# Kernel tuning notes

Measured on AMD Instinct MI355X. Metric: run time of the kernel, lower is better.

The kernel has to match this reference:

```python
import jax, jax.numpy as jnp
import numpy as np

N, B, C, H = 2048, 2, 1024, 16
HD = C // H


def setup_inputs() -> dict:
    key = jax.random.key(0)
    ks = jax.random.split(key, 11)
    s = 0.02
    return {
        "query": jax.random.normal(ks[0], (N, B, C), jnp.float32),
        "key": jax.random.normal(ks[1], (N, B, C), jnp.float32),
        "value": jax.random.normal(ks[2], (B, N, C), jnp.float32),
        "num_heads": H,
        "Wq": jax.random.normal(ks[3], (C, C), jnp.float32) * s,
        "bq": jnp.zeros((C,), jnp.float32),
        "Wk": jax.random.normal(ks[4], (C, HD), jnp.float32) * s,
        "bk": jnp.zeros((HD,), jnp.float32),
        "Wv": jax.random.normal(ks[5], (C, HD), jnp.float32) * s,
        "bv": jnp.zeros((HD,), jnp.float32),
        "Wp": jax.random.normal(ks[6], (C, C), jnp.float32) * s,
        "bp": jnp.zeros((C,), jnp.float32),
    }


def reference(query, key, value, num_heads, Wq, bq, Wk, bk, Wv, bv, Wp, bp):
    # query/key arrive seq-first (N,B,C); permute to batch-first as in torch code
    k_in = jnp.transpose(key, (1, 0, 2))    # (B, Nk, C)
    q_in = jnp.transpose(query, (1, 0, 2))  # (B, Nq, C)
    Bsz, Nq, Cd = q_in.shape
    hd = Cd // num_heads
    scale = hd ** -0.5

    # shared single K/V head (MQA)
    k = k_in @ Wk + bk                      # (B, Nk, hd)
    v = value @ Wv + bv                     # (B, Nk, hd)
    q = (q_in @ Wq + bq).reshape(Bsz, Nq, num_heads, hd)
    q = jnp.transpose(q, (0, 2, 1, 3)) * scale  # (B, H, Nq, hd)

    attn = jnp.einsum('bhqd,bkd->bhqk', q, k)   # (B, H, Nq, Nk)
    attn = jax.nn.softmax(attn, axis=-1)
    x = jnp.einsum('bhqk,bkd->bhqd', attn, v)   # (B, H, Nq, hd)
    x = jnp.transpose(x, (0, 2, 1, 3)).reshape(Bsz, Nq, Cd)
    x = x @ Wp + bp
    return jnp.transpose(x, (1, 0, 2))          # (Nq, B, C)
```

## Files before the change

### kernel.cpp

```cpp
#include <hip/hip_runtime.h>
#include <hip/hip_bf16.h>

#define DI __device__ __forceinline__

typedef float f32x4 __attribute__((ext_vector_type(4)));
typedef float f32x16 __attribute__((ext_vector_type(16)));
typedef short s16x8 __attribute__((ext_vector_type(8)));
typedef unsigned short u16x4 __attribute__((ext_vector_type(4)));
typedef unsigned long long u64;


DI unsigned short f2bf(float x) {
  union { float f; unsigned u; } v; v.f = x;
  unsigned r = 0x7fffu + ((v.u >> 16) & 1u);
  return (unsigned short)((v.u + r) >> 16);
}

DI unsigned cvtpk(float lo, float hi) {
  unsigned u;
  asm("v_cvt_pk_bf16_f32 %0, %1, %2" : "=v"(u) : "v"(lo), "v"(hi));
  return u;
}

DI float max3f(float a, float b, float c) {
  float d;
  asm("v_max3_f32 %0, %1, %2, %3" : "=v"(d) : "v"(a), "v"(b), "v"(c));
  return d;
}

DI f32x16 zero16() {
  f32x16 z;
#pragma unroll
  for (int i = 0; i < 16; ++i) z[i] = 0.f;
  return z;
}

DI float max16_3(const f32x16& a) {
  float m0 = max3f(a[0], a[1], a[2]);
  float m1 = max3f(a[3], a[4], a[5]);
  float m2 = max3f(a[6], a[7], a[8]);
  float m3 = max3f(a[9], a[10], a[11]);
  float m4 = max3f(a[12], a[13], a[14]);
  float n0 = max3f(m0, m1, m2);
  float n1 = max3f(m3, m4, a[15]);
  return fmaxf(n0, n1);
}

DI float sum16(const f32x16& a) {
  float s0 = a[0] + a[1],  s1 = a[2] + a[3];
  float s2 = a[4] + a[5],  s3 = a[6] + a[7];
  float s4 = a[8] + a[9],  s5 = a[10] + a[11];
  float s6 = a[12] + a[13], s7 = a[14] + a[15];
  s0 += s1; s2 += s3; s4 += s5; s6 += s7;
  return (s0 + s2) + (s4 + s6);
}

DI void gll16(const void* g, void* l) {
  __builtin_amdgcn_global_load_lds(
      (const __attribute__((address_space(1))) void*)g,
      (__attribute__((address_space(3))) void*)l, 16, 0, 0);
}

DI f32x16 mfma32(s16x8 a, s16x8 b, f32x16 c) {
  return __builtin_amdgcn_mfma_f32_32x32x16_bf16(a, b, c, 0, 0, 0);
}

DI f32x4 mfma16(s16x8 a, s16x8 b, f32x4 c) {
  return __builtin_amdgcn_mfma_f32_16x16x32_bf16(a, b, c, 0, 0, 0);
}

__global__ __launch_bounds__(256) void prep_kernel(
    const float* __restrict__ q, unsigned short* __restrict__ qbf,
    const float* __restrict__ Wq, const float* __restrict__ Wk,
    const float* __restrict__ Wv, const float* __restrict__ Wp,
    unsigned short* __restrict__ WqT, unsigned short* __restrict__ WkT,
    unsigned short* __restrict__ WvT, unsigned short* __restrict__ WpT)
{
  int bid = blockIdx.x;
  if (bid < 2048) {
    int gid = bid * 256 + threadIdx.x;
    int row = gid >> 7;
    int c8 = (gid & 127) << 3;
    int b = row >> 11, n = row & 2047;
    size_t soff = ((size_t)n * 2 + b) * 1024 + c8;
    f32x4 v0 = *(const f32x4*)(q + soff);
    f32x4 v1 = *(const f32x4*)(q + soff + 4);
    union { unsigned u[4]; s16x8 v; } x;
    x.u[0] = cvtpk(v0.x, v0.y); x.u[1] = cvtpk(v0.z, v0.w);
    x.u[2] = cvtpk(v1.x, v1.y); x.u[3] = cvtpk(v1.z, v1.w);
    *(s16x8*)(qbf + (size_t)row * 1024 + c8) = x.v;
    return;
  }
  int wb = bid - 2048;
  const float* W; unsigned short* WT; int Ncols; int base;
  if (wb < 512)       { W = Wq; WT = WqT; Ncols = 1024; base = wb; }
  else if (wb < 1024) { W = Wp; WT = WpT; Ncols = 1024; base = wb - 512; }
  else if (wb < 1056) { W = Wk; WT = WkT; Ncols = 64;   base = wb - 1024; }
  else                { W = Wv; WT = WvT; Ncols = 64;   base = wb - 1056; }
  int nb = base >> 5, kb = base & 31;
  int n = nb * 64 + (threadIdx.x & 63);
  int k = kb * 32 + (threadIdx.x >> 6) * 8;
  float f[8];
#pragma unroll
  for (int i = 0; i < 8; ++i) f[i] = W[(size_t)(k + i) * Ncols + n];
  union { unsigned u[4]; s16x8 v; } x;
#pragma unroll
  for (int i = 0; i < 4; ++i) x.u[i] = cvtpk(f[2 * i], f[2 * i + 1]);
  *(s16x8*)(WT + (size_t)n * 1024 + k) = x.v;
}

template<int MODE>
DI void gemm16_body(const unsigned short* __restrict__ A,
                    const unsigned short* __restrict__ Bt,
                    const float* __restrict__ bias, void* __restrict__ Cpv,
                    float scale, int bx, int by,
                    unsigned short* As, unsigned short* Bs)
{
  const int tid = threadIdx.x;
  const int lane = tid & 63, wave = tid >> 6;
  const int l16 = lane & 15, kq = lane >> 4;
  const int wr = wave >> 1, wc = wave & 1;
  const int row0 = bx * 128;
  const int col0 = by * 64;

  f32x4 acc[4][2];
#pragma unroll
  for (int mi = 0; mi < 4; ++mi)
#pragma unroll
    for (int nj = 0; nj < 2; ++nj) acc[mi][nj] = f32x4{0.f, 0.f, 0.f, 0.f};

  auto STAGE = [&](int bf, int kt) {
    const int k0 = kt * 64;
    char* Ad = (char*)As + bf * 16384;
    char* Bd = (char*)Bs + bf * 8192;
#pragma unroll
    for (int i = 0; i < 4; ++i) {
      int o = i * 4096 + tid * 16;
      int r = o >> 7, c = (o & 127) >> 1;
      gll16(A + (size_t)(row0 + r) * 1024 + k0 + c, Ad + i * 4096 + wave * 1024);
    }
#pragma unroll
    for (int i = 0; i < 2; ++i) {
      int o = i * 4096 + tid * 16;
      int r = o >> 7, c = (o & 127) >> 1;
      gll16(Bt + (size_t)(col0 + r) * 1024 + k0 + c, Bd + i * 4096 + wave * 1024);
    }
  };

  STAGE(0, 0);
  __syncthreads();
  int cur = 0;
  for (int kt = 0; kt < 16; ++kt) {
    if (kt + 1 < 16) STAGE(cur ^ 1, kt + 1);
#pragma unroll
    for (int ks = 0; ks < 2; ++ks) {
      s16x8 af[4]; s16x8 bf2[2];
#pragma unroll
      for (int mi = 0; mi < 4; ++mi)
        af[mi] = *(const s16x8*)(As + cur * 8192 + (wr * 64 + mi * 16 + l16) * 64 + ks * 32 + kq * 8);
#pragma unroll
      for (int nj = 0; nj < 2; ++nj)
        bf2[nj] = *(const s16x8*)(Bs + cur * 4096 + (wc * 32 + nj * 16 + l16) * 64 + ks * 32 + kq * 8);
#pragma unroll
      for (int mi = 0; mi < 4; ++mi)
#pragma unroll
        for (int nj = 0; nj < 2; ++nj)
          acc[mi][nj] = mfma16(af[mi], bf2[nj], acc[mi][nj]);
    }
    __syncthreads();
    cur ^= 1;
  }

#pragma unroll
  for (int mi = 0; mi < 4; ++mi)
#pragma unroll
  for (int nj = 0; nj < 2; ++nj) {
    int col = col0 + wc * 32 + nj * 16 + l16;
    int rowb = row0 + wr * 64 + mi * 16 + kq * 4;
    float bv = bias[col];
#pragma unroll
    for (int r = 0; r < 4; ++r) {
      int row = rowb + r;
      float val = acc[mi][nj][r] + bv;
      if constexpr (MODE == 0) {
        ((unsigned short*)Cpv)[(size_t)row * 1024 + col] = f2bf(val * scale);
      } else {
        ((float*)Cpv)[(size_t)(row & 2047) * 2048 + (size_t)(row >> 11) * 1024 + col] = val;
      }
    }
  }
}

DI void gemmkv_body(const float* __restrict__ Akey, const float* __restrict__ Aval,
                    const unsigned short* __restrict__ Wk,
                    const unsigned short* __restrict__ Wv,
                    float* __restrict__ part, int bx, int sel, int bz,
                    unsigned short* As, unsigned short* Bs)
{
  const int tid = threadIdx.x;
  const int lane = tid & 63, wave = tid >> 6;
  const int l16 = lane & 15, kq = lane >> 4;
  const int wr = wave >> 1, wc = wave & 1;
  const float* Af = sel ? Aval : Akey;
  const unsigned short* Bt = sel ? Wv : Wk;
  const int row0 = bx * 64;
  const int kt0 = bz * 4, kt1 = kt0 + 4;

  const int ar = tid >> 2, ac = (tid & 3) * 16;
  const int gm = row0 + ar;
  const size_t grow = sel ? (size_t)gm * 1024
                          : (size_t)((gm & 2047) * 2 + (gm >> 11)) * 1024;

  auto LOADA = [&](int kt, f32x4* a4) {
#pragma unroll
    for (int i = 0; i < 4; ++i)
      a4[i] = *(const f32x4*)(Af + grow + kt * 64 + ac + i * 4);
  };
  auto WRITEA = [&](int bf, const f32x4* a4) {
    union { unsigned u[8]; s16x8 v[2]; } x;
#pragma unroll
    for (int i = 0; i < 4; ++i) {
      x.u[2 * i]     = cvtpk(a4[i].x, a4[i].y);
      x.u[2 * i + 1] = cvtpk(a4[i].z, a4[i].w);
    }
    *(s16x8*)(As + bf * 4096 + ar * 64 + ac)     = x.v[0];
    *(s16x8*)(As + bf * 4096 + ar * 64 + ac + 8) = x.v[1];
  };
  auto STAGEB = [&](int bf, int kt) {
#pragma unroll
    for (int i = 0; i < 2; ++i) {
      int o = i * 4096 + tid * 16;
      int r = o >> 7, c = (o & 127) >> 1;
      gll16(Bt + (size_t)r * 1024 + kt * 64 + c,
            (char*)Bs + bf * 8192 + i * 4096 + wave * 1024);
    }
  };

  f32x4 acc[2][2];
#pragma unroll
  for (int mi = 0; mi < 2; ++mi)
#pragma unroll
    for (int nj = 0; nj < 2; ++nj) acc[mi][nj] = f32x4{0.f, 0.f, 0.f, 0.f};

  f32x4 a4[4];
  LOADA(kt0, a4);
  STAGEB(0, kt0);
  WRITEA(0, a4);
  __syncthreads();
  int cur = 0;
  for (int kt = kt0; kt < kt1; ++kt) {
    if (kt + 1 < kt1) { LOADA(kt + 1, a4); STAGEB(cur ^ 1, kt + 1); }
#pragma unroll
    for (int ks = 0; ks < 2; ++ks) {
      s16x8 af[2]; s16x8 bf2[2];
#pragma unroll
      for (int mi = 0; mi < 2; ++mi)
        af[mi] = *(const s16x8*)(As + cur * 4096 + (wr * 32 + mi * 16 + l16) * 64 + ks * 32 + kq * 8);
#pragma unroll
      for (int nj = 0; nj < 2; ++nj)
        bf2[nj] = *(const s16x8*)(Bs + cur * 4096 + (wc * 32 + nj * 16 + l16) * 64 + ks * 32 + kq * 8);
#pragma unroll
      for (int mi = 0; mi < 2; ++mi)
#pragma unroll
        for (int nj = 0; nj < 2; ++nj)
          acc[mi][nj] = mfma16(af[mi], bf2[nj], acc[mi][nj]);
    }
    if (kt + 1 < kt1) WRITEA(cur ^ 1, a4);
    __syncthreads();
    cur ^= 1;
  }

#pragma unroll
  for (int mi = 0; mi < 2; ++mi)
#pragma unroll
  for (int nj = 0; nj < 2; ++nj) {
    int col = wc * 32 + nj * 16 + l16;
    int rowb = row0 + wr * 32 + mi * 16 + kq * 4;
#pragma unroll
    for (int r = 0; r < 4; ++r)
      part[(((size_t)bz * 2 + sel) * 4096 + rowb + r) * 64 + col] = acc[mi][nj][r];
  }
}

__global__ __launch_bounds__(256) void gemmqkv_kernel(
    const unsigned short* __restrict__ qbf, const unsigned short* __restrict__ WqT,
    const float* __restrict__ bq, unsigned short* __restrict__ qproj, float qscale,
    const float* __restrict__ key, const float* __restrict__ value,
    const unsigned short* __restrict__ WkT, const unsigned short* __restrict__ WvT,
    float* __restrict__ part)
{
  __shared__ __align__(16) unsigned short SMEM[24576];
  int bid = blockIdx.x;
  if (bid < 512) {
    gemm16_body<0>(qbf, WqT, bq, qproj, qscale, bid & 31, bid >> 5,
                   SMEM, SMEM + 16384);
  } else {
    int idx = bid - 512;
    gemmkv_body(key, value, WkT, WvT, part, idx & 63, (idx >> 6) & 1, idx >> 7,
                SMEM, SMEM + 8192);
  }
}

__global__ __launch_bounds__(256) void gemmout_kernel(
    const unsigned short* __restrict__ A, const unsigned short* __restrict__ Bt,
    const float* __restrict__ bias, float* __restrict__ Cpv)
{
  __shared__ __align__(16) unsigned short SMEM[24576];
  gemm16_body<2>(A, Bt, bias, (void*)Cpv, 1.0f, blockIdx.x, blockIdx.y,
                 SMEM, SMEM + 16384);
}

__global__ __launch_bounds__(256) void kvreduce_kernel(
    const float* __restrict__ part, const float* __restrict__ bk,
    const float* __restrict__ bv, unsigned short* __restrict__ kproj,
    unsigned short* __restrict__ vprojT)
{
  int gid = blockIdx.x * 256 + threadIdx.x;
  int kv = gid >> 18;
  int rem = gid & 262143;
  int row = rem >> 6, col = rem & 63;
  float s = 0.f;
#pragma unroll
  for (int z = 0; z < 4; ++z)
    s += part[(((size_t)z * 2 + kv) * 4096 + row) * 64 + col];
  s += (kv ? bv : bk)[col];
  if (kv == 0)
    kproj[(size_t)row * 64 + col] = f2bf(s);
  else
    vprojT[(size_t)(row >> 11) * 131072 + (size_t)col * 2048 + (row & 2047)] = f2bf(s);
}

__global__ __launch_bounds__(512, 4) void attn_kernel(
    const unsigned short* __restrict__ qp, const unsigned short* __restrict__ kp,
    const unsigned short* __restrict__ vpt, unsigned short* __restrict__ xout)
{
  constexpr int KSTR = 72;
  __shared__ unsigned short SM[36864];
#define KBUF(c, hh) (SM + ((c) * 2 + (hh)) * (64 * KSTR))
#define VBUF(c, hh) (SM + 18432 + ((c) * 2 + (hh)) * (64 * KSTR))

  const int tid = threadIdx.x;
  const int lane = tid & 63, wave = tid >> 6;
  const int lq = lane & 31, hi = lane >> 5;
  const int qsub = wave & 3, half = wave >> 2;
  const int b = blockIdx.y >> 4, h = blockIdx.y & 15;
  const int q0 = blockIdx.x * 128 + qsub * 32;
  const size_t qrow = (size_t)(b * 2048 + q0 + lq);

  s16x8 qf[4];
#pragma unroll
  for (int s = 0; s < 4; ++s)
    qf[s] = *(const s16x8*)(qp + qrow * 1024 + h * 64 + s * 16 + hi * 8);

  f32x16 xacc0 = zero16(), xacc1 = zero16();
  float mrun = -1e30f, ssum = 0.f;

  const unsigned short* kb = kp + (size_t)b * (2048 * 64);
  const unsigned short* vb = vpt + (size_t)b * (64 * 2048);

  const int srow = tid >> 3;
  const int scol = (tid & 7) * 8;

  s16x8 kA, kB, vA, vB;
  {
    kA = *(const s16x8*)(kb + (size_t)srow * 64 + scol);
    kB = *(const s16x8*)(kb + (size_t)(16 * 64 + srow) * 64 + scol);
    vA = *(const s16x8*)(vb + (size_t)srow * 2048 + scol);
    vB = *(const s16x8*)(vb + (size_t)srow * 2048 + 16 * 64 + scol);
    *(s16x8*)(KBUF(0, 0) + srow * KSTR + scol) = kA;
    *(s16x8*)(KBUF(0, 1) + srow * KSTR + scol) = kB;
    *(s16x8*)(VBUF(0, 0) + srow * KSTR + scol) = vA;
    *(s16x8*)(VBUF(0, 1) + srow * KSTR + scol) = vB;
  }
  int cur = 0;

  for (int it = 0; it < 16; ++it) {
    __syncthreads();
    if (it + 1 < 16) {
      kA = *(const s16x8*)(kb + (size_t)((it + 1) * 64 + srow) * 64 + scol);
      kB = *(const s16x8*)(kb + (size_t)((it + 17) * 64 + srow) * 64 + scol);
      vA = *(const s16x8*)(vb + (size_t)srow * 2048 + (it + 1) * 64 + scol);
      vB = *(const s16x8*)(vb + (size_t)srow * 2048 + (it + 17) * 64 + scol);
    }
    const unsigned short* Kc = KBUF(cur, half);
    const unsigned short* Vc = VBUF(cur, half);

    f32x16 sacc0 = zero16(), sacc1 = zero16();
    __builtin_amdgcn_s_setprio(1);
#pragma unroll
    for (int s = 0; s < 4; ++s) {
      int c = s * 16 + hi * 8;
      s16x8 kf0 = *(const s16x8*)(Kc + lq * KSTR + c);
      s16x8 kf1 = *(const s16x8*)(Kc + (32 + lq) * KSTR + c);
      sacc0 = mfma32(kf0, qf[s], sacc0);
      sacc1 = mfma32(kf1, qf[s], sacc1);
    }
    __builtin_amdgcn_s_setprio(0);

    float tm = fmaxf(max16_3(sacc0), max16_3(sacc1));
    tm = fmaxf(tm, __shfl_xor(tm, 32));
    if (!__all(tm <= mrun + 8.f)) {
      float mnew = fmaxf(mrun, tm);
      float alpha = __builtin_amdgcn_exp2f(mrun - mnew);
      ssum *= alpha;
#pragma unroll
      for (int e = 0; e < 16; ++e) { xacc0[e] *= alpha; xacc1[e] *= alpha; }
      mrun = mnew;
    }
    f32x16 p0, p1;
#pragma unroll
    for (int e = 0; e < 16; ++e) p0[e] = __builtin_amdgcn_exp2f(sacc0[e] - mrun);
#pragma unroll
    for (int e = 0; e < 16; ++e) p1[e] = __builtin_amdgcn_exp2f(sacc1[e] - mrun);
    float tsum = sum16(p0) + sum16(p1);
    tsum += __shfl_xor(tsum, 32);
    ssum += tsum;

    s16x8 pb[4];
#pragma unroll
    for (int grp = 0; grp < 4; ++grp) {
      const f32x16& pp = (grp < 2) ? p0 : p1;
      const int eb = (grp & 1) * 8;
      unsigned A  = cvtpk(pp[eb + 0], pp[eb + 1]);
      unsigned Bw = cvtpk(pp[eb + 2], pp[eb + 3]);
      unsigned Cw = cvtpk(pp[eb + 4], pp[eb + 5]);
      unsigned Dw = cvtpk(pp[eb + 6], pp[eb + 7]);
      unsigned rA = (unsigned)__shfl_xor((int)(hi ? A : Cw), 32);
      unsigned rB = (unsigned)__shfl_xor((int)(hi ? Bw : Dw), 32);
      union { unsigned u[4]; s16x8 v; } pk_;
      pk_.u[0] = hi ? rA : A;
      pk_.u[1] = hi ? rB : Bw;
      pk_.u[2] = hi ? Cw : rA;
      pk_.u[3] = hi ? Dw : rB;
      pb[grp] = pk_.v;
    }

    __builtin_amdgcn_s_setprio(1);
#pragma unroll
    for (int kvs = 0; kvs < 4; ++kvs) {
      int c = kvs * 16 + hi * 8;
      s16x8 vf0 = *(const s16x8*)(Vc + lq * KSTR + c);
      s16x8 vf1 = *(const s16x8*)(Vc + (32 + lq) * KSTR + c);
      xacc0 = mfma32(vf0, pb[kvs], xacc0);
      xacc1 = mfma32(vf1, pb[kvs], xacc1);
    }
    __builtin_amdgcn_s_setprio(0);

    if (it + 1 < 16) {
      *(s16x8*)(KBUF(cur ^ 1, 0) + srow * KSTR + scol) = kA;
      *(s16x8*)(KBUF(cur ^ 1, 1) + srow * KSTR + scol) = kB;
      *(s16x8*)(VBUF(cur ^ 1, 0) + srow * KSTR + scol) = vA;
      *(s16x8*)(VBUF(cur ^ 1, 1) + srow * KSTR + scol) = vB;
      cur ^= 1;
    }
  }

  __syncthreads();
  float* msc = (float*)SM;
  const int mi_ = (qsub * 64 + lane) * 37;
  if (half == 1) {
#pragma unroll
    for (int e = 0; e < 16; ++e) { msc[mi_ + e] = xacc0[e]; msc[mi_ + 16 + e] = xacc1[e]; }
    msc[mi_ + 32] = mrun;
    msc[mi_ + 33] = ssum;
  }
  __syncthreads();
  if (half == 0) {
    float pm = msc[mi_ + 32], ps = msc[mi_ + 33];
    float mf = fmaxf(mrun, pm);
    float aa = __builtin_amdgcn_exp2f(mrun - mf);
    float bb = __builtin_amdgcn_exp2f(pm - mf);
    float inv = 1.0f / (ssum * aa + ps * bb);
#pragma unroll
    for (int dj = 0; dj < 2; ++dj) {
      const f32x16 xa = dj ? xacc1 : xacc0;
#pragma unroll
      for (int g = 0; g < 4; ++g) {
        u16x4 o4;
#pragma unroll
        for (int r = 0; r < 4; ++r) {
          int e = g * 4 + r;
          float merged = xa[e] * aa + msc[mi_ + dj * 16 + e] * bb;
          o4[r] = f2bf(merged * inv);
        }
        int d0 = dj * 32 + 8 * g + 4 * hi;
        *(u16x4*)(xout + qrow * 1024 + h * 64 + d0) = o4;
      }
    }
  }
#undef KBUF
#undef VBUF
}

extern "C" void kernel_launch(void* const* d_in, const int* in_sizes, int n_in,
                              void* d_out, int out_size, void* d_ws, size_t ws_size,
                              hipStream_t stream)
{
  const float* query = (const float*)d_in[0];
  const float* key   = (const float*)d_in[1];
  const float* value = (const float*)d_in[2];
  const float* Wq = (const float*)d_in[4];
  const float* bq = (const float*)d_in[5];
  const float* Wk = (const float*)d_in[6];
  const float* bk = (const float*)d_in[7];
  const float* Wv = (const float*)d_in[8];
  const float* bv = (const float*)d_in[9];
  const float* Wp = (const float*)d_in[10];
  const float* bp = (const float*)d_in[11];

  char* ws = (char*)d_ws;
  unsigned short* WqT    = (unsigned short*)(ws);
  unsigned short* WpT    = (unsigned short*)(ws + (2u << 20));
  unsigned short* WkT    = (unsigned short*)(ws + (4u << 20));
  unsigned short* WvT    = (unsigned short*)(ws + (4u << 20) + (128u << 10));
  unsigned short* kproj  = (unsigned short*)(ws + (5u << 20));
  unsigned short* vprojT = (unsigned short*)(ws + (5u << 20) + (512u << 10));
  unsigned short* qproj  = (unsigned short*)(ws + (6u << 20));
  unsigned short* xbuf   = (unsigned short*)(ws + (15u << 20));
  float*          part   = (float*)xbuf;
  unsigned short* qbf    = (unsigned short*)d_out;

  prep_kernel<<<dim3(3136), 256, 0, stream>>>(
      query, qbf, Wq, Wk, Wv, Wp, WqT, WkT, WvT, WpT);

  const float qscale = 0.18033688011112042f;
  gemmqkv_kernel<<<dim3(1024), 256, 0, stream>>>(
      qbf, WqT, bq, qproj, qscale, key, value, WkT, WvT, part);
  kvreduce_kernel<<<dim3(2048), 256, 0, stream>>>(part, bk, bv, kproj, vprojT);
  attn_kernel<<<dim3(16, 32), 512, 0, stream>>>(qproj, kproj, vprojT, xbuf);
  gemmout_kernel<<<dim3(32, 16), 256, 0, stream>>>(xbuf, WpT, bp, (float*)d_out);
}
```

Measured before the change: 104.3 us.

## Drop split-K for K/V projection and fuse bias/convert epilogue, removing reduce kernel

The K/V projection blocks now run the full K=1024 reduction themselves instead of splitting it four ways and summing partials in a separate kvreduce kernel. They add bias and write bf16 kproj/vprojT directly, which removes one launch and the fp32 partial-buffer round trip. The cost is fewer, longer KV blocks (128 instead of 512), which may leave the tail of the fused QKV launch underfilled. In attention, the cross-half shuffle of the row sum is deferred until after the loop, saving one shuffle per iteration.

```diff
diff --git a/kernel.cpp b/kernel.cpp
--- a/kernel.cpp
+++ b/kernel.cpp
@@ -194,7 +194,10 @@
 DI void gemmkv_body(const float* __restrict__ Akey, const float* __restrict__ Aval,
                     const unsigned short* __restrict__ Wk,
                     const unsigned short* __restrict__ Wv,
-                    float* __restrict__ part, int bx, int sel, int bz,
+                    const float* __restrict__ bk, const float* __restrict__ bv,
+                    unsigned short* __restrict__ kproj,
+                    unsigned short* __restrict__ vprojT,
+                    int bx, int sel,
                     unsigned short* As, unsigned short* Bs)
 {
   const int tid = threadIdx.x;
@@ -204,7 +207,6 @@
   const float* Af = sel ? Aval : Akey;
   const unsigned short* Bt = sel ? Wv : Wk;
   const int row0 = bx * 64;
-  const int kt0 = bz * 4, kt1 = kt0 + 4;
 
   const int ar = tid >> 2, ac = (tid & 3) * 16;
   const int gm = row0 + ar;
@@ -243,13 +245,13 @@
     for (int nj = 0; nj < 2; ++nj) acc[mi][nj] = f32x4{0.f, 0.f, 0.f, 0.f};
 
   f32x4 a4[4];
-  LOADA(kt0, a4);
-  STAGEB(0, kt0);
+  LOADA(0, a4);
+  STAGEB(0, 0);
   WRITEA(0, a4);
   __syncthreads();
   int cur = 0;
-  for (int kt = kt0; kt < kt1; ++kt) {
-    if (kt + 1 < kt1) { LOADA(kt + 1, a4); STAGEB(cur ^ 1, kt + 1); }
+  for (int kt = 0; kt < 16; ++kt) {
+    if (kt + 1 < 16) { LOADA(kt + 1, a4); STAGEB(cur ^ 1, kt + 1); }
 #pragma unroll
     for (int ks = 0; ks < 2; ++ks) {
       s16x8 af[2]; s16x8 bf2[2];
@@ -265,20 +267,28 @@
         for (int nj = 0; nj < 2; ++nj)
           acc[mi][nj] = mfma16(af[mi], bf2[nj], acc[mi][nj]);
     }
-    if (kt + 1 < kt1) WRITEA(cur ^ 1, a4);
+    if (kt + 1 < 16) WRITEA(cur ^ 1, a4);
     __syncthreads();
     cur ^= 1;
   }
 
+  const float* bias = sel ? bv : bk;
 #pragma unroll
   for (int mi = 0; mi < 2; ++mi)
 #pragma unroll
   for (int nj = 0; nj < 2; ++nj) {
     int col = wc * 32 + nj * 16 + l16;
     int rowb = row0 + wr * 32 + mi * 16 + kq * 4;
-#pragma unroll
-    for (int r = 0; r < 4; ++r)
-      part[(((size_t)bz * 2 + sel) * 4096 + rowb + r) * 64 + col] = acc[mi][nj][r];
+    float bb = bias[col];
+#pragma unroll
+    for (int r = 0; r < 4; ++r) {
+      int row = rowb + r;
+      float val = acc[mi][nj][r] + bb;
+      if (sel == 0)
+        kproj[(size_t)row * 64 + col] = f2bf(val);
+      else
+        vprojT[(size_t)(row >> 11) * 131072 + (size_t)col * 2048 + (row & 2047)] = f2bf(val);
+    }
   }
 }
 
@@ -287,7 +297,8 @@
     const float* __restrict__ bq, unsigned short* __restrict__ qproj, float qscale,
     const float* __restrict__ key, const float* __restrict__ value,
     const unsigned short* __restrict__ WkT, const unsigned short* __restrict__ WvT,
-    float* __restrict__ part)
+    const float* __restrict__ bk, const float* __restrict__ bv,
+    unsigned short* __restrict__ kproj, unsigned short* __restrict__ vprojT)
 {
   __shared__ __align__(16) unsigned short SMEM[24576];
   int bid = blockIdx.x;
@@ -296,8 +307,8 @@
                    SMEM, SMEM + 16384);
   } else {
     int idx = bid - 512;
-    gemmkv_body(key, value, WkT, WvT, part, idx & 63, (idx >> 6) & 1, idx >> 7,
-                SMEM, SMEM + 8192);
+    gemmkv_body(key, value, WkT, WvT, bk, bv, kproj, vprojT,
+                idx & 63, idx >> 6, SMEM, SMEM + 8192);
   }
 }
 
@@ -308,26 +319,6 @@
   __shared__ __align__(16) unsigned short SMEM[24576];
   gemm16_body<2>(A, Bt, bias, (void*)Cpv, 1.0f, blockIdx.x, blockIdx.y,
                  SMEM, SMEM + 16384);
-}
-
-__global__ __launch_bounds__(256) void kvreduce_kernel(
-    const float* __restrict__ part, const float* __restrict__ bk,
-    const float* __restrict__ bv, unsigned short* __restrict__ kproj,
-    unsigned short* __restrict__ vprojT)
-{
-  int gid = blockIdx.x * 256 + threadIdx.x;
-  int kv = gid >> 18;
-  int rem = gid & 262143;
-  int row = rem >> 6, col = rem & 63;
-  float s = 0.f;
-#pragma unroll
-  for (int z = 0; z < 4; ++z)
-    s += part[(((size_t)z * 2 + kv) * 4096 + row) * 64 + col];
-  s += (kv ? bv : bk)[col];
-  if (kv == 0)
-    kproj[(size_t)row * 64 + col] = f2bf(s);
-  else
-    vprojT[(size_t)(row >> 11) * 131072 + (size_t)col * 2048 + (row & 2047)] = f2bf(s);
 }
 
 __global__ __launch_bounds__(512, 4) void attn_kernel(
@@ -412,9 +403,7 @@
     for (int e = 0; e < 16; ++e) p0[e] = __builtin_amdgcn_exp2f(sacc0[e] - mrun);
 #pragma unroll
     for (int e = 0; e < 16; ++e) p1[e] = __builtin_amdgcn_exp2f(sacc1[e] - mrun);
-    float tsum = sum16(p0) + sum16(p1);
-    tsum += __shfl_xor(tsum, 32);
-    ssum += tsum;
+    ssum += sum16(p0) + sum16(p1);
 
     s16x8 pb[4];
 #pragma unroll
@@ -454,6 +443,7 @@
       cur ^= 1;
     }
   }
+  ssum += __shfl_xor(ssum, 32);
 
   __syncthreads();
   float* msc = (float*)SM;
@@ -517,16 +507,14 @@
   unsigned short* vprojT = (unsigned short*)(ws + (5u << 20) + (512u << 10));
   unsigned short* qproj  = (unsigned short*)(ws + (6u << 20));
   unsigned short* xbuf   = (unsigned short*)(ws + (15u << 20));
-  float*          part   = (float*)xbuf;
   unsigned short* qbf    = (unsigned short*)d_out;
 
   prep_kernel<<<dim3(3136), 256, 0, stream>>>(
       query, qbf, Wq, Wk, Wv, Wp, WqT, WkT, WvT, WpT);
 
   const float qscale = 0.18033688011112042f;
-  gemmqkv_kernel<<<dim3(1024), 256, 0, stream>>>(
-      qbf, WqT, bq, qproj, qscale, key, value, WkT, WvT, part);
-  kvreduce_kernel<<<dim3(2048), 256, 0, stream>>>(part, bk, bv, kproj, vprojT);
+  gemmqkv_kernel<<<dim3(640), 256, 0, stream>>>(
+      qbf, WqT, bq, qproj, qscale, key, value, WkT, WvT, bk, bv, kproj, vprojT);
   attn_kernel<<<dim3(16, 32), 512, 0, stream>>>(qproj, kproj, vprojT, xbuf);
   gemmout_kernel<<<dim3(32, 16), 256, 0, stream>>>(xbuf, WpT, bp, (float*)d_out);
 }
```

Result: slower. 108.5 us (+4.0%).
